# Kernel optimization log

Measured on AMD Instinct MI355X. Metric: run time of the kernel, lower is better.

The kernel has to match this reference:

```python
import jax, jax.numpy as jnp
import numpy as np

B, T, C = 2, 2048, 2048
N_HEAD, N_KV_HEAD = 16, 4
HEAD_DIM = C // N_HEAD  # 128
EPS = 1e-6


def rms_norm(x):
    # no learned scale, normalize over head_dim (last axis)
    return x * jax.lax.rsqrt(jnp.mean(jnp.square(x), axis=-1, keepdims=True) + EPS)


def apply_rotary_emb(x, cos, sin):
    # x: [B, T, H, D]; cos/sin: [T, D/2]  (rotate-half RoPE)
    x1, x2 = jnp.split(x, 2, axis=-1)
    c = cos[None, :, None, :]
    s = sin[None, :, None, :]
    return jnp.concatenate([x1 * c - x2 * s, x1 * s + x2 * c], axis=-1)


def setup_inputs() -> dict:
    key = jax.random.key(0)
    ks = jax.random.split(key, 6)
    x = jax.random.normal(ks[0], (B, T, C), dtype=jnp.float32)
    # real rotary tables: theta = 10000^{-2i/D}
    inv_freq = 1.0 / (10000.0 ** (jnp.arange(0, HEAD_DIM, 2, dtype=jnp.float32) / HEAD_DIM))
    angles = jnp.arange(T, dtype=jnp.float32)[:, None] * inv_freq[None, :]  # [T, D/2]
    cos, sin = jnp.cos(angles), jnp.sin(angles)
    std = 0.02
    Wq = jax.random.normal(ks[1], (C, N_HEAD * HEAD_DIM), dtype=jnp.float32) * std
    Wk = jax.random.normal(ks[2], (C, N_KV_HEAD * HEAD_DIM), dtype=jnp.float32) * std
    Wv = jax.random.normal(ks[3], (C, N_KV_HEAD * HEAD_DIM), dtype=jnp.float32) * std
    Wp = jax.random.normal(ks[4], (C, C), dtype=jnp.float32) * std
    return {"x": x, "cos": cos, "sin": sin, "Wq": Wq, "Wk": Wk, "Wv": Wv, "Wp": Wp}


def reference(x, cos, sin, Wq, Wk, Wv, Wp):
    Bx, Tx, Cx = x.shape
    q = (x @ Wq).reshape(Bx, Tx, N_HEAD, HEAD_DIM)
    k = (x @ Wk).reshape(Bx, Tx, N_KV_HEAD, HEAD_DIM)
    v = (x @ Wv).reshape(Bx, Tx, N_KV_HEAD, HEAD_DIM)
    q = rms_norm(apply_rotary_emb(q, cos, sin))
    k = rms_norm(apply_rotary_emb(k, cos, sin))
    # module scales q by 1/sqrt(D) AND nn.dot_product_attention scales again
    q = q * (1.0 / jnp.sqrt(HEAD_DIM))
    # GQA head repeat
    n_rep = N_HEAD // N_KV_HEAD
    k = jnp.repeat(k, n_rep, axis=2)  # [B, T, H, D]
    v = jnp.repeat(v, n_rep, axis=2)
    scores = jnp.einsum("bthd,bshd->bhts", q, k) / jnp.sqrt(jnp.asarray(HEAD_DIM, x.dtype))
    causal = jnp.tril(jnp.ones((Tx, Tx), dtype=bool))  # key <= query
    scores = jnp.where(causal[None, None, :, :], scores, jnp.finfo(scores.dtype).min)
    probs = jax.nn.softmax(scores, axis=-1)
    y = jnp.einsum("bhts,bshd->bthd", probs, v).reshape(Bx, Tx, Cx)
    return y @ Wp
```

## Files before the change

kernel.cpp:

```cpp
#include <hip/hip_runtime.h>
#include <hip/hip_bf16.h>
#include <math.h>

#define B_  2
#define T_  2048
#define C_  2048
#define NH_ 16
#define NKV_ 4
#define HD_ 128
#define NREP_ (NH_/NKV_)

#define QKVLD 3072
#define KOFF  2048
#define VOFF  2560

#define QSCALE 0.01127105500694502f

typedef __bf16 bf16x8 __attribute__((ext_vector_type(8)));
typedef float  f32x4  __attribute__((ext_vector_type(4)));
typedef float  f32x16 __attribute__((ext_vector_type(16)));

__device__ inline void gload_lds16(const void* g, void* l) {
    __builtin_amdgcn_global_load_lds((const __attribute__((address_space(1))) void*)g,
                                     (__attribute__((address_space(3))) void*)l, 16, 0, 0);
}

__global__ __launch_bounds__(256) void cast_bf16(const float* __restrict__ src,
                                                 __bf16* __restrict__ dst)
{
    size_t i = ((size_t)blockIdx.x * 256 + threadIdx.x) * 8;
    float4 a = *(const float4*)&src[i];
    float4 b = *(const float4*)&src[i + 4];
    union { __bf16 h[8]; uint4 u; } pk;
    pk.h[0] = (__bf16)a.x; pk.h[1] = (__bf16)a.y; pk.h[2] = (__bf16)a.z; pk.h[3] = (__bf16)a.w;
    pk.h[4] = (__bf16)b.x; pk.h[5] = (__bf16)b.y; pk.h[6] = (__bf16)b.z; pk.h[7] = (__bf16)b.w;
    *(uint4*)&dst[i] = pk.u;
}

__global__ __launch_bounds__(256) void wtrans_qkv(const float* __restrict__ Wq,
                                                  const float* __restrict__ Wk,
                                                  const float* __restrict__ Wv,
                                                  __bf16* __restrict__ dst)
{
    __shared__ float tl[32][33];
    int ct = blockIdx.x;
    int k0 = blockIdx.y * 32;
    const float* src;
    int ncols, c0, dr0;
    if (ct < 64)      { src = Wq; ncols = 2048; c0 = ct * 32;        dr0 = ct * 32; }
    else if (ct < 80) { src = Wk; ncols = 512;  c0 = (ct - 64) * 32; dr0 = KOFF + (ct - 64) * 32; }
    else              { src = Wv; ncols = 512;  c0 = (ct - 80) * 32; dr0 = VOFF + (ct - 80) * 32; }

    int tid = threadIdx.x;
    int r  = tid >> 3;
    int c4 = (tid & 7) * 4;
    float4 v = *(const float4*)&src[(size_t)(k0 + r) * ncols + c0 + c4];
    tl[r][c4] = v.x; tl[r][c4 + 1] = v.y; tl[r][c4 + 2] = v.z; tl[r][c4 + 3] = v.w;
    __syncthreads();
    union { __bf16 h[4]; uint2 u; } pk;
#pragma unroll
    for (int j = 0; j < 4; ++j) pk.h[j] = (__bf16)tl[c4 + j][r];
    *(uint2*)&dst[(size_t)(dr0 + r) * 2048 + k0 + c4] = pk.u;
}

__global__ __launch_bounds__(256) void wtrans(const float* __restrict__ src,
                                              __bf16* __restrict__ dst, int ncols)
{
    __shared__ float tl[32][33];
    int n0 = blockIdx.x * 32;
    int k0 = blockIdx.y * 32;
    int tid = threadIdx.x;
    int r  = tid >> 3;
    int c4 = (tid & 7) * 4;
    float4 v = *(const float4*)&src[(size_t)(k0 + r) * ncols + n0 + c4];
    tl[r][c4] = v.x; tl[r][c4 + 1] = v.y; tl[r][c4 + 2] = v.z; tl[r][c4 + 3] = v.w;
    __syncthreads();
    union { __bf16 h[4]; uint2 u; } pk;
#pragma unroll
    for (int j = 0; j < 4; ++j) pk.h[j] = (__bf16)tl[c4 + j][r];
    *(uint2*)&dst[(size_t)(n0 + r) * 2048 + k0 + c4] = pk.u;
}

template<typename TOUT>
__global__ __launch_bounds__(256) void gemm_bt(const __bf16* __restrict__ A,
                                               const __bf16* __restrict__ Bt,
                                               TOUT* __restrict__ C,
                                               int M, int N, int K, int ldc)
{
    __shared__ __bf16 As[2][128 * 32];
    __shared__ __bf16 Bs[2][128 * 32];

    const int tid  = threadIdx.x;
    const int wv   = tid >> 6;
    const int lane = tid & 63;
    const int grp  = lane >> 4;
    const int id16 = lane & 15;
    const int wr   = wv >> 1;
    const int wc   = wv & 1;

    const int row0 = blockIdx.y * 128;
    const int col0 = blockIdx.x * 128;

    const int sm = tid >> 2;
    const int sk = (tid & 3) << 3;

    const __bf16* ga0 = A  + (size_t)(row0 + sm) * K + sk;
    const __bf16* ga1 = A  + (size_t)(row0 + 64 + sm) * K + sk;
    const __bf16* gb0 = Bt + (size_t)(col0 + sm) * K + sk;
    const __bf16* gb1 = Bt + (size_t)(col0 + 64 + sm) * K + sk;

    f32x4 acc[4][4];
    const f32x4 fz = {0.f, 0.f, 0.f, 0.f};
#pragma unroll
    for (int i = 0; i < 4; ++i)
#pragma unroll
        for (int j = 0; j < 4; ++j) acc[i][j] = fz;

    const int nk = K >> 5;

    {
        __bf16* a0 = &As[0][wv << 9];
        __bf16* b0 = &Bs[0][wv << 9];
        gload_lds16(ga0, a0);
        gload_lds16(ga1, a0 + 2048);
        gload_lds16(gb0, b0);
        gload_lds16(gb1, b0 + 2048);
    }

    for (int kt = 0; kt < nk; ++kt) {
        const int bufc = kt & 1;
        asm volatile("s_waitcnt vmcnt(0)" ::: "memory");
        __syncthreads();

        if (kt + 1 < nk) {
            const int kb = (kt + 1) << 5;
            __bf16* a0 = &As[1 - bufc][wv << 9];
            __bf16* b0 = &Bs[1 - bufc][wv << 9];
            gload_lds16(ga0 + kb, a0);
            gload_lds16(ga1 + kb, a0 + 2048);
            gload_lds16(gb0 + kb, b0);
            gload_lds16(gb1 + kb, b0 + 2048);
        }

        bf16x8 af[4], bfr[4];
#pragma unroll
        for (int i = 0; i < 4; ++i)
            af[i] = *(const bf16x8*)&As[bufc][((wr << 6) + (i << 4) + id16) * 32 + (grp << 3)];
#pragma unroll
        for (int j = 0; j < 4; ++j)
            bfr[j] = *(const bf16x8*)&Bs[bufc][((wc << 6) + (j << 4) + id16) * 32 + (grp << 3)];
#pragma unroll
        for (int i = 0; i < 4; ++i)
#pragma unroll
            for (int j = 0; j < 4; ++j)
                acc[i][j] = __builtin_amdgcn_mfma_f32_16x16x32_bf16(af[i], bfr[j], acc[i][j], 0, 0, 0);
    }

#pragma unroll
    for (int i = 0; i < 4; ++i) {
        int gr = row0 + (wr << 6) + (i << 4) + (grp << 2);
#pragma unroll
        for (int j = 0; j < 4; ++j) {
            int gc = col0 + (wc << 6) + (j << 4) + id16;
#pragma unroll
            for (int r = 0; r < 4; ++r) {
                if constexpr (sizeof(TOUT) == 4)
                    C[(size_t)(gr + r) * ldc + gc] = acc[i][j][r];
                else
                    C[(size_t)(gr + r) * ldc + gc] = (TOUT)acc[i][j][r];
            }
        }
    }
}

__global__ __launch_bounds__(256) void rope_rms_b(__bf16* __restrict__ base,
                                                  const float* __restrict__ cosb,
                                                  const float* __restrict__ sinb,
                                                  int nheads, float scale)
{
    int wid  = blockIdx.x * 4 + (threadIdx.x >> 6);
    int lane = threadIdx.x & 63;
    int bt = wid / nheads;
    int hd = wid % nheads;
    int t  = bt % T_;

    __bf16* p = base + (size_t)bt * QKVLD + hd * HD_;
    float c = cosb[t * 64 + lane];
    float s = sinb[t * 64 + lane];
    float x1 = (float)p[lane];
    float x2 = (float)p[lane + 64];
    float r1 = x1 * c - x2 * s;
    float r2 = x1 * s + x2 * c;
    float ss = r1 * r1 + r2 * r2;
#pragma unroll
    for (int off = 32; off; off >>= 1) ss += __shfl_xor(ss, off, 64);
    float inv = rsqrtf(ss * (1.f / 128.f) + 1e-6f) * scale;
    p[lane]      = (__bf16)(r1 * inv);
    p[lane + 64] = (__bf16)(r2 * inv);
}

__global__ __launch_bounds__(256) void vtrans(const __bf16* __restrict__ qkv,
                                              __bf16* __restrict__ vt)
{
    __shared__ __bf16 tl[32][HD_ + 8];
    int bx  = blockIdx.x;
    int st  = bx & 63;
    int bkv = bx >> 6;
    int b = bkv >> 2, kv = bkv & 3;
    int s0 = st << 5;
    int tid = threadIdx.x;
    {
        int s = tid >> 3;
        int d = (tid & 7) << 4;
        const __bf16* src = qkv + (size_t)(b * T_ + s0 + s) * QKVLD + VOFF + kv * HD_ + d;
        *(bf16x8*)&tl[s][d]     = *(const bf16x8*)src;
        *(bf16x8*)&tl[s][d + 8] = *(const bf16x8*)(src + 8);
    }
    __syncthreads();
    {
        int d  = tid >> 1;
        int sh = (tid & 1) << 4;
        __bf16 tmp[16];
#pragma unroll
        for (int j = 0; j < 16; ++j) tmp[j] = tl[sh + j][d];
        __bf16* dst = vt + ((size_t)(b * NKV_ + kv) * HD_ + d) * T_ + s0 + sh;
        *(bf16x8*)dst       = *(bf16x8*)&tmp[0];
        *(bf16x8*)(dst + 8) = *(bf16x8*)&tmp[8];
    }
}

__global__ __launch_bounds__(256, 2) void attn32(const __bf16* __restrict__ qkv,
                                                 const __bf16* __restrict__ vbT,
                                                 __bf16* __restrict__ y,
                                                 float* __restrict__ pOA,
                                                 float* __restrict__ pOB,
                                                 float* __restrict__ pLA,
                                                 float* __restrict__ pLB)
{
    __shared__ __bf16 Ks[2][64 * 128];
    __shared__ __bf16 Vs[2][64 * 128];

    const int tid  = threadIdx.x;
    const int wv   = tid >> 6;
    const int lane = tid & 63;
    const int l31  = lane & 31;
    const int h32  = lane >> 5;

    const int bx   = blockIdx.x;
    const int bh   = bx & 31;
    const int role = (bx >> 5) & 1;
    const int p    = bx >> 6;
    const int b    = bh >> 4;
    const int h    = bh & 15;
    const int kv   = h >> 2;
    const int slot = p * 32 + bh;

    const int hi  = 15 - p;
    const int lo  = p;
    const int tts = role ? (15 - 2 * p) : 99;

    auto KT = [&](int t) { return role ? (t < tts ? 17 + t : t - tts) : t; };

    int qw0 = hi * 128 + wv * 32;
    int qme = qw0 + l31;

    size_t koff[4], voff[4];
#pragma unroll
    for (int i = 0; i < 4; ++i) {
        int r  = (wv * 4 + i) * 4 + (lane >> 4);
        int c  = lane & 15;
        int cs = c ^ (r & 15);
        koff[i] = (size_t)r * (QKVLD * 2) + (size_t)cs * 16;
        int d   = r + ((cs >> 3) << 6);
        voff[i] = (size_t)d * (T_ * 2) + (size_t)(cs & 7) * 16;
    }
    const char* kg = (const char*)(qkv + (size_t)b * T_ * QKVLD + KOFF + kv * HD_);
    const char* vg = (const char*)(vbT + ((size_t)(b * NKV_ + kv) * HD_) * T_);

    bf16x8 qf[8], qf2[8];
    {
        const __bf16* qp = qkv + (size_t)(b * T_ + hi * 128 + wv * 32 + l31) * QKVLD + h * HD_ + h32 * 8;
#pragma unroll
        for (int s = 0; s < 8; ++s) qf[s] = *(const bf16x8*)(qp + s * 16);
        const __bf16* qp2 = qkv + (size_t)(b * T_ + lo * 128 + wv * 32 + l31) * QKVLD + h * HD_ + h32 * 8;
#pragma unroll
        for (int s = 0; s < 8; ++s) qf2[s] = *(const bf16x8*)(qp2 + s * 16);
    }

    f32x16 o[4];
#pragma unroll
    for (int dt = 0; dt < 4; ++dt)
#pragma unroll
        for (int r = 0; r < 16; ++r) o[dt][r] = 0.f;
    float l_p = 0.f;

#define STORE_PARTIAL(PO, PL)                                                   \
    {                                                                           \
        float lsum = l_p + __shfl_xor(l_p, 32, 64);                             \
        int qloc = wv * 32 + l31;                                               \
        float* po = (PO) + ((size_t)slot * 128 + qloc) * 128;                   \
        _Pragma("unroll")                                                       \
        for (int dt = 0; dt < 4; ++dt)                                          \
            _Pragma("unroll")                                                   \
            for (int g = 0; g < 4; ++g) {                                       \
                float4 f = {o[dt][4 * g + 0], o[dt][4 * g + 1],                 \
                            o[dt][4 * g + 2], o[dt][4 * g + 3]};                \
                *(float4*)&po[dt * 32 + 8 * g + 4 * h32] = f;                   \
            }                                                                   \
        if (h32 == 0) (PL)[slot * 128 + qloc] = lsum;                           \
    }

    {
        int kt0 = KT(0);
        const char* kp = kg + (size_t)kt0 * (64 * QKVLD * 2);
        const char* vp = vg + (size_t)kt0 * (64 * 2);
        __bf16* kl = &Ks[0][(wv * 4) * 512];
        __bf16* vl = &Vs[0][(wv * 4) * 512];
#pragma unroll
        for (int i = 0; i < 4; ++i) gload_lds16(kp + koff[i], kl + i * 512);
#pragma unroll
        for (int i = 0; i < 4; ++i) gload_lds16(vp + voff[i], vl + i * 512);
    }

    for (int tt = 0; tt < 17; ++tt) {
        const int bufc = tt & 1;
        asm volatile("s_waitcnt vmcnt(0)" ::: "memory");
        __syncthreads();

        if (tt + 1 < 17) {
            int kn = KT(tt + 1);
            const char* kp = kg + (size_t)kn * (64 * QKVLD * 2);
            const char* vp = vg + (size_t)kn * (64 * 2);
            __bf16* kl = &Ks[1 - bufc][(wv * 4) * 512];
            __bf16* vl = &Vs[1 - bufc][(wv * 4) * 512];
#pragma unroll
            for (int i = 0; i < 4; ++i) gload_lds16(kp + koff[i], kl + i * 512);
#pragma unroll
            for (int i = 0; i < 4; ++i) gload_lds16(vp + voff[i], vl + i * 512);
        }

        if (role && tt == tts) {
            STORE_PARTIAL(pOB, pLB);
#pragma unroll
            for (int dt = 0; dt < 4; ++dt)
#pragma unroll
                for (int r = 0; r < 16; ++r) o[dt][r] = 0.f;
            l_p = 0.f;
#pragma unroll
            for (int s = 0; s < 8; ++s) qf[s] = qf2[s];
            qw0 = lo * 128 + wv * 32;
            qme = qw0 + l31;
        }

        const int s0 = KT(tt) << 6;
        if (s0 > qw0 + 31) continue;

        f32x16 S0, S1;
#pragma unroll
        for (int r = 0; r < 16; ++r) { S0[r] = 0.f; S1[r] = 0.f; }
        const __bf16* Kb = Ks[bufc];
        __builtin_amdgcn_s_setprio(1);
#pragma unroll
        for (int s = 0; s < 8; ++s) {
            int ch = s * 2 + h32;
            bf16x8 kf0 = *(const bf16x8*)&Kb[l31 * 128 + ((ch ^ (l31 & 15)) << 3)];
            bf16x8 kf1 = *(const bf16x8*)&Kb[(32 + l31) * 128 + ((ch ^ (l31 & 15)) << 3)];
            S0 = __builtin_amdgcn_mfma_f32_32x32x16_bf16(kf0, qf[s], S0, 0, 0, 0);
            S1 = __builtin_amdgcn_mfma_f32_32x32x16_bf16(kf1, qf[s], S1, 0, 0, 0);
        }
        __builtin_amdgcn_s_setprio(0);

        const bool domask = (s0 + 63 > qw0);
        uint w[16];
#pragma unroll
        for (int i = 0; i < 8; ++i) {
            const int r0 = 2 * i;
            float e0 = exp2f(S0[r0]);
            float e1 = exp2f(S0[r0 + 1]);
            if (domask) {
                int k0 = s0 + (r0 & 3) + 8 * (r0 >> 2) + 4 * h32;
                if (k0     > qme) e0 = 0.f;
                if (k0 + 1 > qme) e1 = 0.f;
            }
            l_p += e0 + e1;
            union { __bf16 h2[2]; uint u; } pk;
            pk.h2[0] = (__bf16)e0; pk.h2[1] = (__bf16)e1;
            w[i] = pk.u;
        }
#pragma unroll
        for (int i = 0; i < 8; ++i) {
            const int r0 = 2 * i;
            float e0 = exp2f(S1[r0]);
            float e1 = exp2f(S1[r0 + 1]);
            if (domask) {
                int k0 = s0 + 32 + (r0 & 3) + 8 * (r0 >> 2) + 4 * h32;
                if (k0     > qme) e0 = 0.f;
                if (k0 + 1 > qme) e1 = 0.f;
            }
            l_p += e0 + e1;
            union { __bf16 h2[2]; uint u; } pk;
            pk.h2[0] = (__bf16)e0; pk.h2[1] = (__bf16)e1;
            w[8 + i] = pk.u;
        }

        uint sw[16];
#pragma unroll
        for (int i = 0; i < 16; ++i) sw[i] = (uint)__shfl_xor((int)w[i], 32, 64);

        union U8 { uint u[4]; bf16x8 v; };
        bf16x8 pf[4];
#pragma unroll
        for (int ks = 0; ks < 4; ++ks) {
            const int bsel = ((ks >> 1) << 3) + ((ks & 1) << 2);
            U8 t;
            if (h32 == 0) {
                t.u[0] = w[bsel];      t.u[1] = w[bsel + 1];
                t.u[2] = sw[bsel];     t.u[3] = sw[bsel + 1];
            } else {
                t.u[0] = sw[bsel + 2]; t.u[1] = sw[bsel + 3];
                t.u[2] = w[bsel + 2];  t.u[3] = w[bsel + 3];
            }
            pf[ks] = t.v;
        }

        const __bf16* Vb = Vs[bufc];
        __builtin_amdgcn_s_setprio(1);
#pragma unroll
        for (int dt = 0; dt < 4; ++dt) {
            const int vrow = ((dt & 1) << 5) + l31;
            const int cb   = (dt >> 1) << 3;
#pragma unroll
            for (int ks = 0; ks < 4; ++ks) {
                int ch = cb + ks * 2 + h32;
                bf16x8 vf = *(const bf16x8*)&Vb[vrow * 128 + ((ch ^ (vrow & 15)) << 3)];
                o[dt] = __builtin_amdgcn_mfma_f32_32x32x16_bf16(vf, pf[ks], o[dt], 0, 0, 0);
            }
        }
        __builtin_amdgcn_s_setprio(0);
    }

    if (role == 0) {
        STORE_PARTIAL(pOA, pLA);
    } else {
        float l  = l_p + __shfl_xor(l_p, 32, 64);
        float inv = 1.f / l;
        __bf16* yp = y + (size_t)(b * T_ + qw0 + l31) * C_ + h * HD_;
#pragma unroll
        for (int dt = 0; dt < 4; ++dt)
#pragma unroll
            for (int g = 0; g < 4; ++g) {
                union { __bf16 h4[4]; uint2 u; } pk;
#pragma unroll
                for (int e = 0; e < 4; ++e) pk.h4[e] = (__bf16)(o[dt][4 * g + e] * inv);
                *(uint2*)&yp[dt * 32 + 8 * g + 4 * h32] = pk.u;
            }
    }
#undef STORE_PARTIAL
}

__global__ __launch_bounds__(256) void attn_combine(const float* __restrict__ pOA,
                                                    const float* __restrict__ pOB,
                                                    const float* __restrict__ pLA,
                                                    const float* __restrict__ pLB,
                                                    __bf16* __restrict__ y)
{
    int slot = blockIdx.x;
    int p  = slot >> 5, bh = slot & 31;
    int b  = bh >> 4,   h  = bh & 15;
    int hi = 15 - p;
    int t  = threadIdx.x;
    int q  = t >> 1;
    int dh = (t & 1) << 6;

    float inv = 1.f / (pLA[slot * 128 + q] + pLB[slot * 128 + q]);
    size_t base = ((size_t)slot * 128 + q) * 128 + dh;
    __bf16* yp = y + (size_t)(b * T_ + hi * 128 + q) * C_ + h * HD_ + dh;
#pragma unroll
    for (int d0 = 0; d0 < 64; d0 += 8) {
        float4 a0 = *(const float4*)&pOA[base + d0];
        float4 a1 = *(const float4*)&pOA[base + d0 + 4];
        float4 b0 = *(const float4*)&pOB[base + d0];
        float4 b1 = *(const float4*)&pOB[base + d0 + 4];
        union { __bf16 h8[8]; uint4 u; } pk;
        pk.h8[0] = (__bf16)((a0.x + b0.x) * inv);
        pk.h8[1] = (__bf16)((a0.y + b0.y) * inv);
        pk.h8[2] = (__bf16)((a0.z + b0.z) * inv);
        pk.h8[3] = (__bf16)((a0.w + b0.w) * inv);
        pk.h8[4] = (__bf16)((a1.x + b1.x) * inv);
        pk.h8[5] = (__bf16)((a1.y + b1.y) * inv);
        pk.h8[6] = (__bf16)((a1.z + b1.z) * inv);
        pk.h8[7] = (__bf16)((a1.w + b1.w) * inv);
        *(uint4*)&yp[d0] = pk.u;
    }
}

extern "C" void kernel_launch(void* const* d_in, const int* in_sizes, int n_in,
                              void* d_out, int out_size, void* d_ws, size_t ws_size,
                              hipStream_t stream)
{
    const float* x    = (const float*)d_in[0];
    const float* cosb = (const float*)d_in[1];
    const float* sinb = (const float*)d_in[2];
    const float* Wq   = (const float*)d_in[3];
    const float* Wk   = (const float*)d_in[4];
    const float* Wv   = (const float*)d_in[5];
    const float* Wp   = (const float*)d_in[6];
    float* out = (float*)d_out;

    const int M = B_ * T_;

    char* w = (char*)d_ws;
    __bf16* xb    = (__bf16*)w;  w += (size_t)M * C_ * 2;
    __bf16* qkv   = (__bf16*)w;  w += (size_t)M * QKVLD * 2;
    __bf16* wqkvT = (__bf16*)w;  w += (size_t)QKVLD * C_ * 2;
    __bf16* wpT   = (__bf16*)w;  w += (size_t)C_ * C_ * 2;
    __bf16* vt    = (__bf16*)w;  w += (size_t)M * NKV_ * HD_ * 2;
    __bf16* y     = (__bf16*)w;  w += (size_t)M * C_ * 2;
    float*  pOB   = (float*)w;
    float*  pOA   = (float*)xb;
    float*  pLA   = (float*)wqkvT;
    float*  pLB   = pLA + 8 * 32 * 128;

    cast_bf16<<<(M * C_) / 2048, 256, 0, stream>>>(x, xb);
    wtrans_qkv<<<dim3(96, C_ / 32), 256, 0, stream>>>(Wq, Wk, Wv, wqkvT);
    wtrans<<<dim3(C_ / 32, C_ / 32), 256, 0, stream>>>(Wp, wpT, C_);

    gemm_bt<__bf16><<<dim3(QKVLD / 128, M / 128), 256, 0, stream>>>(xb, wqkvT, qkv, M, QKVLD, C_, QKVLD);

    rope_rms_b<<<(M * NH_) / 4, 256, 0, stream>>>(qkv, cosb, sinb, NH_, QSCALE);
    rope_rms_b<<<(M * NKV_) / 4, 256, 0, stream>>>(qkv + KOFF, cosb, sinb, NKV_, 1.0f);

    vtrans<<<B_ * NKV_ * (T_ / 32), 256, 0, stream>>>(qkv, vt);

    attn32<<<512, 256, 0, stream>>>(qkv, vt, y, pOA, pOB, pLA, pLB);
    attn_combine<<<256, 256, 0, stream>>>(pOA, pOB, pLA, pLB, y);

    gemm_bt<float><<<dim3(C_ / 128, M / 128), 256, 0, stream>>>(y, wpT, out, M, C_, C_, C_);
}
```

Measured before the change: 327.1 us.

## Split attention head dim across blocks and shrink KV tiles to 32 keys

Splits each attention work item across two blocks that each compute half of the head output dimension (dh), doubling the grid to 1024 blocks. Key tiles shrink from 64 to 32 keys, with smaller LDS buffers and half the accumulator registers, and occupancy is raised to 4 blocks per CU. The second Q fragment is reloaded from global memory at the role switch instead of being held in registers. This adds parallelism and occupancy, but both halves recompute the same QK^T scores and softmax, which doubles score work. It also doubles the number of loop iterations and barriers.

Result: slower. 362.2 us (+10.7%).

```diff
diff --git a/kernel.cpp b/kernel.cpp
--- a/kernel.cpp
+++ b/kernel.cpp
@@ -229,7 +229,7 @@
     }
 }
 
-__global__ __launch_bounds__(256, 2) void attn32(const __bf16* __restrict__ qkv,
+__global__ __launch_bounds__(256, 4) void attn32(const __bf16* __restrict__ qkv,
                                                  const __bf16* __restrict__ vbT,
                                                  __bf16* __restrict__ y,
                                                  float* __restrict__ pOA,
@@ -237,8 +237,8 @@
                                                  float* __restrict__ pLA,
                                                  float* __restrict__ pLB)
 {
-    __shared__ __bf16 Ks[2][64 * 128];
-    __shared__ __bf16 Vs[2][64 * 128];
+    __shared__ __bf16 Ks[2][32 * 128];
+    __shared__ __bf16 Vs[2][16 * 128];
 
     const int tid  = threadIdx.x;
     const int wv   = tid >> 6;
@@ -248,8 +248,9 @@
 
     const int bx   = blockIdx.x;
     const int bh   = bx & 31;
-    const int role = (bx >> 5) & 1;
-    const int p    = bx >> 6;
+    const int dh   = (bx >> 5) & 1;
+    const int role = (bx >> 6) & 1;
+    const int p    = bx >> 7;
     const int b    = bh >> 4;
     const int h    = bh & 15;
     const int kv   = h >> 2;
@@ -257,39 +258,47 @@
 
     const int hi  = 15 - p;
     const int lo  = p;
-    const int tts = role ? (15 - 2 * p) : 99;
-
-    auto KT = [&](int t) { return role ? (t < tts ? 17 + t : t - tts) : t; };
+    const int NHt = 64 - 4 * p;
+    const int tts = role ? (NHt - 34) : 99;
+
+    auto KT = [&](int t) { return role ? (t < tts ? 34 + t : t - tts) : t; };
 
     int qw0 = hi * 128 + wv * 32;
     int qme = qw0 + l31;
 
-    size_t koff[4], voff[4];
-#pragma unroll
-    for (int i = 0; i < 4; ++i) {
-        int r  = (wv * 4 + i) * 4 + (lane >> 4);
+    uint koff0, koff1, voff;
+    {
+        int r0 = wv * 8 + (lane >> 4);
         int c  = lane & 15;
-        int cs = c ^ (r & 15);
-        koff[i] = (size_t)r * (QKVLD * 2) + (size_t)cs * 16;
-        int d   = r + ((cs >> 3) << 6);
-        voff[i] = (size_t)d * (T_ * 2) + (size_t)(cs & 7) * 16;
+        koff0 = (uint)(r0 * (QKVLD * 2) + ((c ^ (r0 & 15)) << 4));
+        int r1 = r0 + 4;
+        koff1 = (uint)(r1 * (QKVLD * 2) + ((c ^ (r1 & 15)) << 4));
+        int rv = wv * 4 + (lane >> 4);
+        int cs = c ^ rv;
+        voff = (uint)((dh * 64 + rv + ((cs >> 2) << 4)) * (T_ * 2) + ((cs & 3) << 4));
     }
     const char* kg = (const char*)(qkv + (size_t)b * T_ * QKVLD + KOFF + kv * HD_);
     const char* vg = (const char*)(vbT + ((size_t)(b * NKV_ + kv) * HD_) * T_);
 
-    bf16x8 qf[8], qf2[8];
-    {
-        const __bf16* qp = qkv + (size_t)(b * T_ + hi * 128 + wv * 32 + l31) * QKVLD + h * HD_ + h32 * 8;
-#pragma unroll
-        for (int s = 0; s < 8; ++s) qf[s] = *(const bf16x8*)(qp + s * 16);
-        const __bf16* qp2 = qkv + (size_t)(b * T_ + lo * 128 + wv * 32 + l31) * QKVLD + h * HD_ + h32 * 8;
-#pragma unroll
-        for (int s = 0; s < 8; ++s) qf2[s] = *(const bf16x8*)(qp2 + s * 16);
-    }
-
-    f32x16 o[4];
-#pragma unroll
-    for (int dt = 0; dt < 4; ++dt)
+#define STAGE(BUF, KN)                                                        \
+    {                                                                         \
+        const char* kp = kg + (size_t)(KN) * (32 * QKVLD * 2);                \
+        const char* vp = vg + (size_t)(KN) * (32 * 2);                        \
+        __bf16* kl = &Ks[BUF][(wv * 8) * 128];                                \
+        gload_lds16(kp + koff0, kl);                                          \
+        gload_lds16(kp + koff1, kl + 512);                                    \
+        gload_lds16(vp + voff, &Vs[BUF][(wv * 4) * 128]);                     \
+    }
+
+    const __bf16* qp  = qkv + (size_t)(b * T_ + hi * 128 + wv * 32 + l31) * QKVLD + h * HD_ + h32 * 8;
+    const __bf16* qp2 = qkv + (size_t)(b * T_ + lo * 128 + wv * 32 + l31) * QKVLD + h * HD_ + h32 * 8;
+    bf16x8 qf[8];
+#pragma unroll
+    for (int s = 0; s < 8; ++s) qf[s] = *(const bf16x8*)(qp + s * 16);
+
+    f32x16 o[2];
+#pragma unroll
+    for (int dt = 0; dt < 2; ++dt)
 #pragma unroll
         for (int r = 0; r < 16; ++r) o[dt][r] = 0.f;
     float l_p = 0.f;
@@ -298,87 +307,66 @@
     {                                                                           \
         float lsum = l_p + __shfl_xor(l_p, 32, 64);                             \
         int qloc = wv * 32 + l31;                                               \
-        float* po = (PO) + ((size_t)slot * 128 + qloc) * 128;                   \
+        float* po = (PO) + ((size_t)slot * 128 + qloc) * 128 + dh * 64;         \
         _Pragma("unroll")                                                       \
-        for (int dt = 0; dt < 4; ++dt)                                          \
+        for (int dt = 0; dt < 2; ++dt)                                          \
             _Pragma("unroll")                                                   \
             for (int g = 0; g < 4; ++g) {                                       \
                 float4 f = {o[dt][4 * g + 0], o[dt][4 * g + 1],                 \
                             o[dt][4 * g + 2], o[dt][4 * g + 3]};                \
                 *(float4*)&po[dt * 32 + 8 * g + 4 * h32] = f;                   \
             }                                                                   \
-        if (h32 == 0) (PL)[slot * 128 + qloc] = lsum;                           \
-    }
-
-    {
-        int kt0 = KT(0);
-        const char* kp = kg + (size_t)kt0 * (64 * QKVLD * 2);
-        const char* vp = vg + (size_t)kt0 * (64 * 2);
-        __bf16* kl = &Ks[0][(wv * 4) * 512];
-        __bf16* vl = &Vs[0][(wv * 4) * 512];
-#pragma unroll
-        for (int i = 0; i < 4; ++i) gload_lds16(kp + koff[i], kl + i * 512);
-#pragma unroll
-        for (int i = 0; i < 4; ++i) gload_lds16(vp + voff[i], vl + i * 512);
-    }
-
-    for (int tt = 0; tt < 17; ++tt) {
+        if (h32 == 0 && dh == 0) (PL)[slot * 128 + qloc] = lsum;                \
+    }
+
+    STAGE(0, KT(0));
+
+    for (int tt = 0; tt < 34; ++tt) {
         const int bufc = tt & 1;
         asm volatile("s_waitcnt vmcnt(0)" ::: "memory");
         __syncthreads();
 
-        if (tt + 1 < 17) {
+        if (tt + 1 < 34) {
             int kn = KT(tt + 1);
-            const char* kp = kg + (size_t)kn * (64 * QKVLD * 2);
-            const char* vp = vg + (size_t)kn * (64 * 2);
-            __bf16* kl = &Ks[1 - bufc][(wv * 4) * 512];
-            __bf16* vl = &Vs[1 - bufc][(wv * 4) * 512];
-#pragma unroll
-            for (int i = 0; i < 4; ++i) gload_lds16(kp + koff[i], kl + i * 512);
-#pragma unroll
-            for (int i = 0; i < 4; ++i) gload_lds16(vp + voff[i], vl + i * 512);
+            STAGE(1 - bufc, kn);
         }
 
         if (role && tt == tts) {
             STORE_PARTIAL(pOB, pLB);
 #pragma unroll
-            for (int dt = 0; dt < 4; ++dt)
+            for (int dt = 0; dt < 2; ++dt)
 #pragma unroll
                 for (int r = 0; r < 16; ++r) o[dt][r] = 0.f;
             l_p = 0.f;
 #pragma unroll
-            for (int s = 0; s < 8; ++s) qf[s] = qf2[s];
+            for (int s = 0; s < 8; ++s) qf[s] = *(const bf16x8*)(qp2 + s * 16);
             qw0 = lo * 128 + wv * 32;
             qme = qw0 + l31;
         }
 
-        const int s0 = KT(tt) << 6;
+        const int s0 = KT(tt) << 5;
         if (s0 > qw0 + 31) continue;
 
-        f32x16 S0, S1;
-#pragma unroll
-        for (int r = 0; r < 16; ++r) { S0[r] = 0.f; S1[r] = 0.f; }
+        f32x16 S;
+#pragma unroll
+        for (int r = 0; r < 16; ++r) S[r] = 0.f;
         const __bf16* Kb = Ks[bufc];
         __builtin_amdgcn_s_setprio(1);
 #pragma unroll
         for (int s = 0; s < 8; ++s) {
-            int ch = s * 2 + h32;
-            bf16x8 kf0 = *(const bf16x8*)&Kb[l31 * 128 + ((ch ^ (l31 & 15)) << 3)];
-            bf16x8 kf1 = *(const bf16x8*)&Kb[(32 + l31) * 128 + ((ch ^ (l31 & 15)) << 3)];
-            S0 = __builtin_amdgcn_mfma_f32_32x32x16_bf16(kf0, qf[s], S0, 0, 0, 0);
-            S1 = __builtin_amdgcn_mfma_f32_32x32x16_bf16(kf1, qf[s], S1, 0, 0, 0);
+            bf16x8 kf = *(const bf16x8*)&Kb[l31 * 128 + (((s * 2 + h32) ^ (l31 & 15)) << 3)];
+            S = __builtin_amdgcn_mfma_f32_32x32x16_bf16(kf, qf[s], S, 0, 0, 0);
         }
         __builtin_amdgcn_s_setprio(0);
 
-        const bool domask = (s0 + 63 > qw0);
-        uint w[16];
+        const bool domask = (s0 + 31 > qw0);
+        uint w[8];
 #pragma unroll
         for (int i = 0; i < 8; ++i) {
-            const int r0 = 2 * i;
-            float e0 = exp2f(S0[r0]);
-            float e1 = exp2f(S0[r0 + 1]);
+            float e0 = exp2f(S[2 * i]);
+            float e1 = exp2f(S[2 * i + 1]);
             if (domask) {
-                int k0 = s0 + (r0 & 3) + 8 * (r0 >> 2) + 4 * h32;
+                int k0 = s0 + 2 * (i & 1) + 8 * (i >> 1) + 4 * h32;
                 if (k0     > qme) e0 = 0.f;
                 if (k0 + 1 > qme) e1 = 0.f;
             }
@@ -387,38 +375,23 @@
             pk.h2[0] = (__bf16)e0; pk.h2[1] = (__bf16)e1;
             w[i] = pk.u;
         }
-#pragma unroll
-        for (int i = 0; i < 8; ++i) {
-            const int r0 = 2 * i;
-            float e0 = exp2f(S1[r0]);
-            float e1 = exp2f(S1[r0 + 1]);
-            if (domask) {
-                int k0 = s0 + 32 + (r0 & 3) + 8 * (r0 >> 2) + 4 * h32;
-                if (k0     > qme) e0 = 0.f;
-                if (k0 + 1 > qme) e1 = 0.f;
-            }
-            l_p += e0 + e1;
-            union { __bf16 h2[2]; uint u; } pk;
-            pk.h2[0] = (__bf16)e0; pk.h2[1] = (__bf16)e1;
-            w[8 + i] = pk.u;
-        }
-
-        uint sw[16];
-#pragma unroll
-        for (int i = 0; i < 16; ++i) sw[i] = (uint)__shfl_xor((int)w[i], 32, 64);
+
+        uint sw[8];
+#pragma unroll
+        for (int i = 0; i < 8; ++i) sw[i] = (uint)__shfl_xor((int)w[i], 32, 64);
 
         union U8 { uint u[4]; bf16x8 v; };
-        bf16x8 pf[4];
-#pragma unroll
-        for (int ks = 0; ks < 4; ++ks) {
-            const int bsel = ((ks >> 1) << 3) + ((ks & 1) << 2);
+        bf16x8 pf[2];
+#pragma unroll
+        for (int ks = 0; ks < 2; ++ks) {
+            const int b4 = 4 * ks;
             U8 t;
             if (h32 == 0) {
-                t.u[0] = w[bsel];      t.u[1] = w[bsel + 1];
-                t.u[2] = sw[bsel];     t.u[3] = sw[bsel + 1];
+                t.u[0] = w[b4];      t.u[1] = w[b4 + 1];
+                t.u[2] = sw[b4];     t.u[3] = sw[b4 + 1];
             } else {
-                t.u[0] = sw[bsel + 2]; t.u[1] = sw[bsel + 3];
-                t.u[2] = w[bsel + 2];  t.u[3] = w[bsel + 3];
+                t.u[0] = sw[b4 + 2]; t.u[1] = sw[b4 + 3];
+                t.u[2] = w[b4 + 2];  t.u[3] = w[b4 + 3];
             }
             pf[ks] = t.v;
         }
@@ -426,13 +399,12 @@
         const __bf16* Vb = Vs[bufc];
         __builtin_amdgcn_s_setprio(1);
 #pragma unroll
-        for (int dt = 0; dt < 4; ++dt) {
-            const int vrow = ((dt & 1) << 5) + l31;
-            const int cb   = (dt >> 1) << 3;
-#pragma unroll
-            for (int ks = 0; ks < 4; ++ks) {
-                int ch = cb + ks * 2 + h32;
-                bf16x8 vf = *(const bf16x8*)&Vb[vrow * 128 + ((ch ^ (vrow & 15)) << 3)];
+        for (int dt = 0; dt < 2; ++dt) {
+            const int rv = l31 & 15;
+            const int gg = dt * 2 + (l31 >> 4);
+#pragma unroll
+            for (int ks = 0; ks < 2; ++ks) {
+                bf16x8 vf = *(const bf16x8*)&Vb[rv * 128 + ((((gg << 2) + (ks << 1) + h32) ^ rv) << 3)];
                 o[dt] = __builtin_amdgcn_mfma_f32_32x32x16_bf16(vf, pf[ks], o[dt], 0, 0, 0);
             }
         }
@@ -444,9 +416,9 @@
     } else {
         float l  = l_p + __shfl_xor(l_p, 32, 64);
         float inv = 1.f / l;
-        __bf16* yp = y + (size_t)(b * T_ + qw0 + l31) * C_ + h * HD_;
-#pragma unroll
-        for (int dt = 0; dt < 4; ++dt)
+        __bf16* yp = y + (size_t)(b * T_ + qw0 + l31) * C_ + h * HD_ + dh * 64;
+#pragma unroll
+        for (int dt = 0; dt < 2; ++dt)
 #pragma unroll
             for (int g = 0; g < 4; ++g) {
                 union { __bf16 h4[4]; uint2 u; } pk;
@@ -456,6 +428,7 @@
             }
     }
 #undef STORE_PARTIAL
+#undef STAGE
 }
 
 __global__ __launch_bounds__(256) void attn_combine(const float* __restrict__ pOA,
@@ -532,7 +505,7 @@
 
     vtrans<<<B_ * NKV_ * (T_ / 32), 256, 0, stream>>>(qkv, vt);
 
-    attn32<<<512, 256, 0, stream>>>(qkv, vt, y, pOA, pOB, pLA, pLB);
+    attn32<<<1024, 256, 0, stream>>>(qkv, vt, y, pOA, pOB, pLA, pLB);
     attn_combine<<<256, 256, 0, stream>>>(pOA, pOB, pLA, pLB, y);
 
     gemm_bt<float><<<dim3(C_ / 128, M / 128), 256, 0, stream>>>(y, wpT, out, M, C_, C_, C_);
```

## Unroll attention tile loop by two, precompute LDS offsets, remap block indices

Applied to the files above, without the earlier changes.

Remaps blockIdx so that blocks sharing a KV head and batch are adjacent in launch order, which is meant to improve L2 reuse of K/V tiles. The K/V tile loop is unrolled by two so the double-buffer index is a compile-time constant. Swizzled LDS byte offsets are precomputed once into off8[] and global offsets are narrowed to 32-bit to cut address arithmetic and VGPR use. The P shuffle now exchanges only the needed half of the words per ks, halving the cross-lane shuffles. Code size grows, and register pressure may shift under the 2-waves launch bound.

After: 326.5 us. No clear change (-0.2%).

```diff
diff --git a/kernel.cpp b/kernel.cpp
--- a/kernel.cpp
+++ b/kernel.cpp
@@ -247,12 +247,14 @@
     const int h32  = lane >> 5;
 
     const int bx   = blockIdx.x;
-    const int bh   = bx & 31;
-    const int role = (bx >> 5) & 1;
-    const int p    = bx >> 6;
-    const int b    = bh >> 4;
-    const int h    = bh & 15;
-    const int kv   = h >> 2;
+    const int b    = (bx >> 2) & 1;
+    const int kv   = bx & 3;
+    const int m    = bx >> 3;
+    const int hh   = m & 3;
+    const int role = (m >> 2) & 1;
+    const int p    = m >> 3;
+    const int h    = kv * 4 + hh;
+    const int bh   = b * 16 + h;
     const int slot = p * 32 + bh;
 
     const int hi  = 15 - p;
@@ -264,18 +266,35 @@
     int qw0 = hi * 128 + wv * 32;
     int qme = qw0 + l31;
 
-    size_t koff[4], voff[4];
+    uint koff[4], voff[4];
 #pragma unroll
     for (int i = 0; i < 4; ++i) {
         int r  = (wv * 4 + i) * 4 + (lane >> 4);
         int c  = lane & 15;
         int cs = c ^ (r & 15);
-        koff[i] = (size_t)r * (QKVLD * 2) + (size_t)cs * 16;
+        koff[i] = (uint)(r * (QKVLD * 2) + cs * 16);
         int d   = r + ((cs >> 3) << 6);
-        voff[i] = (size_t)d * (T_ * 2) + (size_t)(cs & 7) * 16;
+        voff[i] = (uint)(d * (T_ * 2) + (cs & 7) * 16);
     }
     const char* kg = (const char*)(qkv + (size_t)b * T_ * QKVLD + KOFF + kv * HD_);
     const char* vg = (const char*)(vbT + ((size_t)(b * NKV_ + kv) * HD_) * T_);
+
+    uint off8[8];
+#pragma unroll
+    for (int s = 0; s < 8; ++s)
+        off8[s] = (uint)(l31 * 256 + ((((s << 1) + h32) ^ (l31 & 15)) << 4));
+
+#define STAGE(BUF, KN)                                                        \
+    {                                                                         \
+        const char* kp = kg + (size_t)(KN) * (64 * QKVLD * 2);                \
+        const char* vp = vg + (size_t)(KN) * (64 * 2);                        \
+        __bf16* kl = &Ks[BUF][(wv * 4) * 512];                                \
+        __bf16* vl = &Vs[BUF][(wv * 4) * 512];                                \
+        _Pragma("unroll")                                                     \
+        for (int i = 0; i < 4; ++i) gload_lds16(kp + koff[i], kl + i * 512);  \
+        _Pragma("unroll")                                                     \
+        for (int i = 0; i < 4; ++i) gload_lds16(vp + voff[i], vl + i * 512);  \
+    }
 
     bf16x8 qf[8], qf2[8];
     {
@@ -310,134 +329,113 @@
         if (h32 == 0) (PL)[slot * 128 + qloc] = lsum;                           \
     }
 
-    {
-        int kt0 = KT(0);
-        const char* kp = kg + (size_t)kt0 * (64 * QKVLD * 2);
-        const char* vp = vg + (size_t)kt0 * (64 * 2);
-        __bf16* kl = &Ks[0][(wv * 4) * 512];
-        __bf16* vl = &Vs[0][(wv * 4) * 512];
-#pragma unroll
-        for (int i = 0; i < 4; ++i) gload_lds16(kp + koff[i], kl + i * 512);
-#pragma unroll
-        for (int i = 0; i < 4; ++i) gload_lds16(vp + voff[i], vl + i * 512);
-    }
-
-    for (int tt = 0; tt < 17; ++tt) {
-        const int bufc = tt & 1;
-        asm volatile("s_waitcnt vmcnt(0)" ::: "memory");
-        __syncthreads();
-
-        if (tt + 1 < 17) {
-            int kn = KT(tt + 1);
-            const char* kp = kg + (size_t)kn * (64 * QKVLD * 2);
-            const char* vp = vg + (size_t)kn * (64 * 2);
-            __bf16* kl = &Ks[1 - bufc][(wv * 4) * 512];
-            __bf16* vl = &Vs[1 - bufc][(wv * 4) * 512];
-#pragma unroll
-            for (int i = 0; i < 4; ++i) gload_lds16(kp + koff[i], kl + i * 512);
-#pragma unroll
-            for (int i = 0; i < 4; ++i) gload_lds16(vp + voff[i], vl + i * 512);
-        }
-
-        if (role && tt == tts) {
-            STORE_PARTIAL(pOB, pLB);
-#pragma unroll
-            for (int dt = 0; dt < 4; ++dt)
-#pragma unroll
-                for (int r = 0; r < 16; ++r) o[dt][r] = 0.f;
-            l_p = 0.f;
-#pragma unroll
-            for (int s = 0; s < 8; ++s) qf[s] = qf2[s];
-            qw0 = lo * 128 + wv * 32;
-            qme = qw0 + l31;
-        }
-
-        const int s0 = KT(tt) << 6;
-        if (s0 > qw0 + 31) continue;
-
-        f32x16 S0, S1;
-#pragma unroll
-        for (int r = 0; r < 16; ++r) { S0[r] = 0.f; S1[r] = 0.f; }
-        const __bf16* Kb = Ks[bufc];
-        __builtin_amdgcn_s_setprio(1);
-#pragma unroll
-        for (int s = 0; s < 8; ++s) {
-            int ch = s * 2 + h32;
-            bf16x8 kf0 = *(const bf16x8*)&Kb[l31 * 128 + ((ch ^ (l31 & 15)) << 3)];
-            bf16x8 kf1 = *(const bf16x8*)&Kb[(32 + l31) * 128 + ((ch ^ (l31 & 15)) << 3)];
-            S0 = __builtin_amdgcn_mfma_f32_32x32x16_bf16(kf0, qf[s], S0, 0, 0, 0);
-            S1 = __builtin_amdgcn_mfma_f32_32x32x16_bf16(kf1, qf[s], S1, 0, 0, 0);
-        }
-        __builtin_amdgcn_s_setprio(0);
-
-        const bool domask = (s0 + 63 > qw0);
-        uint w[16];
-#pragma unroll
-        for (int i = 0; i < 8; ++i) {
-            const int r0 = 2 * i;
-            float e0 = exp2f(S0[r0]);
-            float e1 = exp2f(S0[r0 + 1]);
-            if (domask) {
-                int k0 = s0 + (r0 & 3) + 8 * (r0 >> 2) + 4 * h32;
-                if (k0     > qme) e0 = 0.f;
-                if (k0 + 1 > qme) e1 = 0.f;
-            }
-            l_p += e0 + e1;
-            union { __bf16 h2[2]; uint u; } pk;
-            pk.h2[0] = (__bf16)e0; pk.h2[1] = (__bf16)e1;
-            w[i] = pk.u;
-        }
-#pragma unroll
-        for (int i = 0; i < 8; ++i) {
-            const int r0 = 2 * i;
-            float e0 = exp2f(S1[r0]);
-            float e1 = exp2f(S1[r0 + 1]);
-            if (domask) {
-                int k0 = s0 + 32 + (r0 & 3) + 8 * (r0 >> 2) + 4 * h32;
-                if (k0     > qme) e0 = 0.f;
-                if (k0 + 1 > qme) e1 = 0.f;
-            }
-            l_p += e0 + e1;
-            union { __bf16 h2[2]; uint u; } pk;
-            pk.h2[0] = (__bf16)e0; pk.h2[1] = (__bf16)e1;
-            w[8 + i] = pk.u;
-        }
-
-        uint sw[16];
-#pragma unroll
-        for (int i = 0; i < 16; ++i) sw[i] = (uint)__shfl_xor((int)w[i], 32, 64);
-
-        union U8 { uint u[4]; bf16x8 v; };
-        bf16x8 pf[4];
-#pragma unroll
-        for (int ks = 0; ks < 4; ++ks) {
-            const int bsel = ((ks >> 1) << 3) + ((ks & 1) << 2);
-            U8 t;
-            if (h32 == 0) {
-                t.u[0] = w[bsel];      t.u[1] = w[bsel + 1];
-                t.u[2] = sw[bsel];     t.u[3] = sw[bsel + 1];
-            } else {
-                t.u[0] = sw[bsel + 2]; t.u[1] = sw[bsel + 3];
-                t.u[2] = w[bsel + 2];  t.u[3] = w[bsel + 3];
-            }
-            pf[ks] = t.v;
-        }
-
-        const __bf16* Vb = Vs[bufc];
-        __builtin_amdgcn_s_setprio(1);
-#pragma unroll
-        for (int dt = 0; dt < 4; ++dt) {
-            const int vrow = ((dt & 1) << 5) + l31;
-            const int cb   = (dt >> 1) << 3;
-#pragma unroll
-            for (int ks = 0; ks < 4; ++ks) {
-                int ch = cb + ks * 2 + h32;
-                bf16x8 vf = *(const bf16x8*)&Vb[vrow * 128 + ((ch ^ (vrow & 15)) << 3)];
-                o[dt] = __builtin_amdgcn_mfma_f32_32x32x16_bf16(vf, pf[ks], o[dt], 0, 0, 0);
-            }
-        }
-        __builtin_amdgcn_s_setprio(0);
-    }
+#define TILE_BODY(TT, BUFC)                                                     \
+    {                                                                           \
+        const int tt_ = (TT);                                                   \
+        asm volatile("s_waitcnt vmcnt(0)" ::: "memory");                        \
+        __syncthreads();                                                        \
+        if (tt_ + 1 < 17) { int kn_ = KT(tt_ + 1); STAGE(1 - (BUFC), kn_); }    \
+        if (role && tt_ == tts) {                                               \
+            STORE_PARTIAL(pOB, pLB);                                            \
+            _Pragma("unroll")                                                   \
+            for (int dt = 0; dt < 4; ++dt)                                      \
+                _Pragma("unroll")                                               \
+                for (int r = 0; r < 16; ++r) o[dt][r] = 0.f;                    \
+            l_p = 0.f;                                                          \
+            _Pragma("unroll")                                                   \
+            for (int s = 0; s < 8; ++s) qf[s] = qf2[s];                         \
+            qw0 = lo * 128 + wv * 32;                                           \
+            qme = qw0 + l31;                                                    \
+        }                                                                       \
+        const int s0 = KT(tt_) << 6;                                            \
+        if (s0 <= qw0 + 31) {                                                   \
+            const char* Kb = (const char*)&Ks[BUFC][0];                         \
+            const char* Vb = (const char*)&Vs[BUFC][0];                         \
+            f32x16 S0, S1;                                                      \
+            _Pragma("unroll")                                                   \
+            for (int r = 0; r < 16; ++r) { S0[r] = 0.f; S1[r] = 0.f; }          \
+            __builtin_amdgcn_s_setprio(1);                                      \
+            _Pragma("unroll")                                                   \
+            for (int s = 0; s < 8; ++s) {                                       \
+                bf16x8 kf0 = *(const bf16x8*)(Kb + off8[s]);                    \
+                bf16x8 kf1 = *(const bf16x8*)(Kb + off8[s] + 8192);             \
+                S0 = __builtin_amdgcn_mfma_f32_32x32x16_bf16(kf0, qf[s], S0, 0, 0, 0); \
+                S1 = __builtin_amdgcn_mfma_f32_32x32x16_bf16(kf1, qf[s], S1, 0, 0, 0); \
+            }                                                                   \
+            __builtin_amdgcn_s_setprio(0);                                      \
+            const bool domask = (s0 + 63 > qw0);                                \
+            uint w[16];                                                         \
+            _Pragma("unroll")                                                   \
+            for (int i = 0; i < 8; ++i) {                                       \
+                const int r0 = 2 * i;                                           \
+                float e0 = exp2f(S0[r0]);                                       \
+                float e1 = exp2f(S0[r0 + 1]);                                   \
+                if (domask) {                                                   \
+                    int k0 = s0 + (r0 & 3) + 8 * (r0 >> 2) + 4 * h32;           \
+                    if (k0     > qme) e0 = 0.f;                                 \
+                    if (k0 + 1 > qme) e1 = 0.f;                                 \
+                }                                                               \
+                l_p += e0 + e1;                                                 \
+                union { __bf16 h2[2]; uint u; } pk;                             \
+                pk.h2[0] = (__bf16)e0; pk.h2[1] = (__bf16)e1;                   \
+                w[i] = pk.u;                                                    \
+            }                                                                   \
+            _Pragma("unroll")                                                   \
+            for (int i = 0; i < 8; ++i) {                                       \
+                const int r0 = 2 * i;                                           \
+                float e0 = exp2f(S1[r0]);                                       \
+                float e1 = exp2f(S1[r0 + 1]);                                   \
+                if (domask) {                                                   \
+                    int k0 = s0 + 32 + (r0 & 3) + 8 * (r0 >> 2) + 4 * h32;      \
+                    if (k0     > qme) e0 = 0.f;                                 \
+                    if (k0 + 1 > qme) e1 = 0.f;                                 \
+                }                                                               \
+                l_p += e0 + e1;                                                 \
+                union { __bf16 h2[2]; uint u; } pk;                             \
+                pk.h2[0] = (__bf16)e0; pk.h2[1] = (__bf16)e1;                   \
+                w[8 + i] = pk.u;                                                \
+            }                                                                   \
+            union U8 { uint u[4]; bf16x8 v; };                                  \
+            bf16x8 pf[4];                                                       \
+            _Pragma("unroll")                                                   \
+            for (int ks = 0; ks < 4; ++ks) {                                    \
+                const int bsel = ((ks >> 1) << 3) + ((ks & 1) << 2);            \
+                uint sa = h32 ? w[bsel]     : w[bsel + 2];                      \
+                uint sb = h32 ? w[bsel + 1] : w[bsel + 3];                      \
+                uint g0 = (uint)__shfl_xor((int)sa, 32, 64);                    \
+                uint g1 = (uint)__shfl_xor((int)sb, 32, 64);                    \
+                U8 t;                                                           \
+                if (h32 == 0) {                                                 \
+                    t.u[0] = w[bsel];     t.u[1] = w[bsel + 1];                 \
+                    t.u[2] = g0;          t.u[3] = g1;                          \
+                } else {                                                        \
+                    t.u[0] = g0;          t.u[1] = g1;                          \
+                    t.u[2] = w[bsel + 2]; t.u[3] = w[bsel + 3];                 \
+                }                                                               \
+                pf[ks] = t.v;                                                   \
+            }                                                                   \
+            __builtin_amdgcn_s_setprio(1);                                      \
+            _Pragma("unroll")                                                   \
+            for (int dt = 0; dt < 4; ++dt) {                                    \
+                const int ab = (dt >> 1) << 2;                                  \
+                const int hf = (dt & 1) * 8192;                                 \
+                _Pragma("unroll")                                               \
+                for (int ks = 0; ks < 4; ++ks) {                                \
+                    bf16x8 vf = *(const bf16x8*)(Vb + off8[ab + ks] + hf);      \
+                    o[dt] = __builtin_amdgcn_mfma_f32_32x32x16_bf16(vf, pf[ks], o[dt], 0, 0, 0); \
+                }                                                               \
+            }                                                                   \
+            __builtin_amdgcn_s_setprio(0);                                      \
+        }                                                                       \
+    }
+
+    STAGE(0, KT(0));
+
+    for (int tt = 0; tt < 16; tt += 2) {
+        TILE_BODY(tt, 0);
+        TILE_BODY(tt + 1, 1);
+    }
+    TILE_BODY(16, 0);
 
     if (role == 0) {
         STORE_PARTIAL(pOA, pLA);
@@ -455,7 +453,9 @@
                 *(uint2*)&yp[dt * 32 + 8 * g + 4 * h32] = pk.u;
             }
     }
+#undef TILE_BODY
 #undef STORE_PARTIAL
+#undef STAGE
 }
 
 __global__ __launch_bounds__(256) void attn_combine(const float* __restrict__ pOA,
```
